# Kernel tuning notes

Hardware: AMD Instinct MI355X
Metric: run time of the kernel (lower is better)

The kernel has to match this reference:

```python
import jax, jax.numpy as jnp
import numpy as np

N = 50000      # num nodes
E = 1600000    # num edges
C = 128        # channels
F = 4          # number of framelet filters
K = 6          # Chebyshev order
S = 1.0        # spectral scale s
APPROX = np.array([[0.3, 0.15, 0.1, 0.075, 0.06, 0.05],
                   [0.6, 0.3, 0.2, 0.15, 0.12, 0.1],
                   [0.9, 0.45, 0.3, 0.225, 0.18, 0.15],
                   [1.2, 0.6, 0.4, 0.3, 0.24, 0.2]], dtype=np.float32)


def setup_inputs() -> dict:
    key = jax.random.key(0)
    ks = jax.random.split(key, 6)
    scale = (2.0 / C) ** 0.5
    return {
        "x_real": jax.random.normal(ks[0], (N, C), jnp.float32),
        "x_imag": jax.random.normal(ks[1], (N, C), jnp.float32),
        "edge_index": jax.random.randint(ks[2], (2, E), 0, N, dtype=jnp.int32),
        "edge_weight": jax.random.uniform(ks[3], (E,), jnp.float32),
        "approx": jnp.asarray(APPROX),
        "theta": jnp.ones((F,), jnp.float32),
        "W_r": jax.random.normal(ks[4], (C, C), jnp.float32) * scale,
        "W_i": jax.random.normal(ks[5], (C, C), jnp.float32) * scale,
        "num_nodes": N,
    }


def _framelet_fwd(x_real, x_imag, edge_index, edge_weight, approx, theta, W_r, W_i, num_nodes):
    row, col = edge_index[0], edge_index[1]
    w = edge_weight / S

    def A_norm(h):  # h: [N, C] real; normalized adjacency propagation
        return jax.ops.segment_sum(w[:, None] * h[col], row, num_segments=num_nodes)

    # Linearity: sum_i theta_i * sum_k approx[i,k] * T_k(x) == sum_k c_k * T_k(x)
    c = theta @ approx  # [K] effective Chebyshev coefficients

    T0r, T0i = x_real, x_imag
    out_r = c[0] * T0r
    out_i = c[0] * T0i
    T1r, T1i = -A_norm(T0r), -A_norm(T0i)
    out_r = out_r + c[1] * T1r
    out_i = out_i + c[1] * T1i
    for ki in range(2, K):
        T2r = -2.0 * A_norm(T1r) - T0r
        T2i = -2.0 * A_norm(T1i) - T0i
        out_r = out_r + c[ki] * T2r
        out_i = out_i + c[ki] * T2i
        T0r, T0i, T1r, T1i = T1r, T1i, T2r, T2i

    # complex linear: (r + i*j) @ (W_r + W_i*j)^T
    yr = out_r @ W_r.T - out_i @ W_i.T
    yi = out_r @ W_i.T + out_i @ W_r.T
    # CSiLU: SiLU applied to real/imag parts independently
    return jnp.stack([jax.nn.silu(yr), jax.nn.silu(yi)])  # [2, N, C]


def reference(x_real, x_imag, edge_index, edge_weight, approx, theta, W_r, W_i, num_nodes):
    return _framelet_fwd(x_real, x_imag, edge_index, edge_weight, approx, theta, W_r, W_i, num_nodes)
```

## Files before the change

### kernel.cpp

```cpp
#include <hip/hip_runtime.h>
#include <hip/hip_fp16.h>
#include <math.h>


#define CH   128
#define NP   128
#define NP4  64
#define RPB  128
#define MAXBUCK 512

typedef _Float16 half8 __attribute__((ext_vector_type(8)));
typedef float f32x4 __attribute__((ext_vector_type(4)));


__global__ __launch_bounds__(256) void bucket_hist_k(
        const int* __restrict__ row, int* __restrict__ bucket_cnt, int E, int nbuck) {
    __shared__ int h[MAXBUCK];
    for (int j = threadIdx.x; j < nbuck; j += 256) h[j] = 0;
    __syncthreads();
    int stride = gridDim.x * 256;
    for (int e = blockIdx.x * 256 + threadIdx.x; e < E; e += stride)
        atomicAdd(&h[row[e] >> 7], 1);
    __syncthreads();
    for (int j = threadIdx.x; j < nbuck; j += 256)
        if (h[j]) atomicAdd(&bucket_cnt[j], h[j]);
}

__global__ __launch_bounds__(512) void bucket_scan_k(
        const int* __restrict__ bucket_cnt, int* __restrict__ bucket_start,
        int* __restrict__ bucket_cursor, int nbuck, int E) {
    __shared__ int sd[MAXBUCK];
    int t = threadIdx.x;
    int v = (t < nbuck) ? bucket_cnt[t] : 0;
    sd[t] = v;
    __syncthreads();
    for (int off = 1; off < MAXBUCK; off <<= 1) {
        int y = (t >= off) ? sd[t - off] : 0;
        __syncthreads();
        sd[t] += y;
        __syncthreads();
    }
    int excl = sd[t] - v;
    if (t < nbuck) { bucket_start[t] = excl; bucket_cursor[t] = excl; }
    if (t == 0) bucket_start[nbuck] = E;
}

__global__ __launch_bounds__(256) void bucket_place_k(
        const int* __restrict__ row, const int* __restrict__ col,
        const float* __restrict__ w, int* __restrict__ bucket_cursor,
        uint2* __restrict__ tmp, int E, int chunk, int nbuck) {
    __shared__ int cnt[MAXBUCK];
    __shared__ int cur[MAXBUCK];
    int e0 = blockIdx.x * chunk;
    int e1 = e0 + chunk; if (e1 > E) e1 = E;
    if (e0 >= E) return;
    for (int j = threadIdx.x; j < nbuck; j += 256) cnt[j] = 0;
    __syncthreads();
    for (int e = e0 + threadIdx.x; e < e1; e += 256)
        atomicAdd(&cnt[row[e] >> 7], 1);
    __syncthreads();
    for (int j = threadIdx.x; j < nbuck; j += 256) {
        int c = cnt[j];
        cur[j] = c ? atomicAdd(&bucket_cursor[j], c) : 0;
    }
    __syncthreads();
    for (int e = e0 + threadIdx.x; e < e1; e += 256) {
        int r = row[e];
        int b = r >> 7;
        int p = atomicAdd(&cur[b], 1);
        uint2 ent;
        ent.x = ((unsigned)(r & (RPB - 1)) << 16) | (unsigned)col[e];
        ent.y = __float_as_uint(w[e]);
        tmp[p] = ent;
    }
}

__global__ __launch_bounds__(256) void csr_build_k(
        const uint2* __restrict__ tmp, const int* __restrict__ bucket_start,
        int* __restrict__ row_start, unsigned* __restrict__ csr4,
        int N, int E, int nbuck) {
    __shared__ int hist[RPB];
    __shared__ int sc[RPB];
    __shared__ int curs[RPB];
    int b = blockIdx.x;
    int t = threadIdx.x;
    int base = bucket_start[b];
    int endp = bucket_start[b + 1];
    if (t < RPB) hist[t] = 0;
    __syncthreads();
    for (int e = base + t; e < endp; e += 256)
        atomicAdd(&hist[tmp[e].x >> 16], 1);
    __syncthreads();
    if (t < RPB) sc[t] = hist[t];
    __syncthreads();
    for (int off = 1; off < RPB; off <<= 1) {
        int y = 0;
        if (t < RPB && t >= off) y = sc[t - off];
        __syncthreads();
        if (t < RPB) sc[t] += y;
        __syncthreads();
    }
    int r0 = b << 7;
    if (t < RPB) {
        int excl = sc[t] - hist[t];
        if (r0 + t < N) row_start[r0 + t] = base + excl;
        curs[t] = base + excl;
    }
    if (b == nbuck - 1 && t == 0) row_start[N] = E;
    __syncthreads();
    for (int e = base + t; e < endp; e += 256) {
        uint2 ent = tmp[e];
        int rl = ent.x >> 16;
        unsigned c = ent.x & 0xffffu;
        float wv = __uint_as_float(ent.y) * (-1.0f / 16.0f);
        int p = atomicAdd(&curs[rl], 1);
        __half hw = __float2half(wv);
        csr4[p] = (c << 16) | (unsigned)__half_as_ushort(hw);
    }
}

__global__ void coef_k(const float* __restrict__ approx, const float* __restrict__ theta,
                       float* cp) {
    int k = threadIdx.x;
    if (k < 6 && blockIdx.x == 0) {
        float s = 0.f;
        for (int f = 0; f < 4; f++) s += theta[f] * approx[f * 6 + k];
        float sc = 1.f;
        for (int j = 0; j < k; j++) sc *= 32.f;
        cp[k] = s * sc;
    }
}

__global__ void convert_x_k(const float2* __restrict__ xr2, const float2* __restrict__ xi2,
                            __half2* __restrict__ xbuf, int total) {
    int idx = blockIdx.x * blockDim.x + threadIdx.x;
    if (idx >= total) return;
    int i = idx >> 7;
    int p = idx & 127;
    float2 v = (p < 64) ? xr2[(size_t)i * 64 + p] : xi2[(size_t)i * 64 + (p - 64)];
    xbuf[idx] = __floats2half2_rn(v.x, v.y);
}

__global__ void build_whT_k(const float* __restrict__ Wr, const float* __restrict__ Wi,
                            _Float16* __restrict__ WhT) {
    int idx = blockIdx.x * 256 + threadIdx.x;
    int j = idx >> 8, k = idx & 255;
    float v;
    if (j < 128) {
        v = (k < 128) ? Wr[j * 128 + k] : -Wi[j * 128 + (k - 128)];
    } else {
        v = (k < 128) ? Wi[(j - 128) * 128 + k] : Wr[(j - 128) * 128 + (k - 128)];
    }
    WhT[idx] = (_Float16)v;
}


__device__ __forceinline__ void unpack4(uint2 v, float& a, float& b, float& c, float& d) {
    __half2 lo = *reinterpret_cast<__half2*>(&v.x);
    __half2 hi = *reinterpret_cast<__half2*>(&v.y);
    float2 f0 = __half22float2(lo);
    float2 f1 = __half22float2(hi);
    a = f0.x; b = f0.y; c = f1.x; d = f1.y;
}

__device__ __forceinline__ void decode(unsigned ent, int& c, float& wv) {
    c = (int)(ent >> 16);
    wv = __half2float(__ushort_as_half((unsigned short)(ent & 0xffffu)));
}

__device__ __forceinline__ void gather_row(
        const uint2* __restrict__ src, const unsigned* __restrict__ csr,
        int beg, int end, int p4,
        float& s0, float& s1, float& s2, float& s3) {
    int e = beg;
    unsigned c0, c1, c2, c3;
    if (e + 4 <= end) { c0 = csr[e]; c1 = csr[e+1]; c2 = csr[e+2]; c3 = csr[e+3]; }
    for (; e + 8 <= end; e += 4) {
        unsigned n0 = csr[e+4], n1 = csr[e+5], n2 = csr[e+6], n3 = csr[e+7];
        int ia, ib, ic, id; float wa, wb, wc, wd;
        decode(c0, ia, wa); decode(c1, ib, wb); decode(c2, ic, wc); decode(c3, id, wd);
        float a0,a1,a2,a3, b0,b1,b2,b3, d0,d1,d2,d3, f0,f1,f2,f3;
        unpack4(src[(size_t)ia * NP4 + p4], a0,a1,a2,a3);
        unpack4(src[(size_t)ib * NP4 + p4], b0,b1,b2,b3);
        unpack4(src[(size_t)ic * NP4 + p4], d0,d1,d2,d3);
        unpack4(src[(size_t)id * NP4 + p4], f0,f1,f2,f3);
        s0 += wa*a0 + wb*b0 + wc*d0 + wd*f0;
        s1 += wa*a1 + wb*b1 + wc*d1 + wd*f1;
        s2 += wa*a2 + wb*b2 + wc*d2 + wd*f2;
        s3 += wa*a3 + wb*b3 + wc*d3 + wd*f3;
        c0 = n0; c1 = n1; c2 = n2; c3 = n3;
    }
    if (e + 4 <= end) {
        int ia, ib, ic, id; float wa, wb, wc, wd;
        decode(c0, ia, wa); decode(c1, ib, wb); decode(c2, ic, wc); decode(c3, id, wd);
        float a0,a1,a2,a3, b0,b1,b2,b3, d0,d1,d2,d3, f0,f1,f2,f3;
        unpack4(src[(size_t)ia * NP4 + p4], a0,a1,a2,a3);
        unpack4(src[(size_t)ib * NP4 + p4], b0,b1,b2,b3);
        unpack4(src[(size_t)ic * NP4 + p4], d0,d1,d2,d3);
        unpack4(src[(size_t)id * NP4 + p4], f0,f1,f2,f3);
        s0 += wa*a0 + wb*b0 + wc*d0 + wd*f0;
        s1 += wa*a1 + wb*b1 + wc*d1 + wd*f1;
        s2 += wa*a2 + wb*b2 + wc*d2 + wd*f2;
        s3 += wa*a3 + wb*b3 + wc*d3 + wd*f3;
        e += 4;
    }
    for (; e < end; e++) {
        int ia; float wa;
        decode(csr[e], ia, wa);
        float a0,a1,a2,a3;
        unpack4(src[(size_t)ia * NP4 + p4], a0,a1,a2,a3);
        s0 += wa*a0; s1 += wa*a1; s2 += wa*a2; s3 += wa*a3;
    }
}

__global__ __launch_bounds__(256) void spmm_first4_k(
        const uint2* __restrict__ xb4,
        const int* __restrict__ row_start, const unsigned* __restrict__ csr,
        const float* __restrict__ cp,
        uint2* __restrict__ t1, float4* __restrict__ acc4, int N) {
    int t = threadIdx.x;
    int rl = t >> 6;
    int p4 = t & 63;
    int i = blockIdx.x * 4 + rl;
    if (i >= N) return;
    int beg = row_start[i], end = row_start[i + 1];
    float s0 = 0.f, s1 = 0.f, s2 = 0.f, s3 = 0.f;
    gather_row(xb4, csr, beg, end, p4, s0, s1, s2, s3);
    s0 *= 0.5f; s1 *= 0.5f; s2 *= 0.5f; s3 *= 0.5f;
    uint2 pk;
    __half2 h0 = __floats2half2_rn(s0, s1);
    __half2 h1 = __floats2half2_rn(s2, s3);
    pk.x = *reinterpret_cast<unsigned*>(&h0);
    pk.y = *reinterpret_cast<unsigned*>(&h1);
    t1[(size_t)i * NP4 + p4] = pk;
    float o0,o1,o2,o3;
    unpack4(xb4[(size_t)i * NP4 + p4], o0,o1,o2,o3);
    float cp0 = cp[0], cp1 = cp[1];
    int half = p4 >> 5, q = p4 & 31;
    float4 a;
    a.x = cp0 * o0 + cp1 * s0;
    a.y = cp0 * o1 + cp1 * s1;
    a.z = cp0 * o2 + cp1 * s2;
    a.w = cp0 * o3 + cp1 * s3;
    acc4[(size_t)half * N * 32 + (size_t)i * 32 + q] = a;
}

__global__ __launch_bounds__(256) void spmm_step4_k(
        const uint2* __restrict__ cur, const uint2* __restrict__ prev,
        const int* __restrict__ row_start, const unsigned* __restrict__ csr,
        const float* __restrict__ cp, int k,
        uint2* __restrict__ dst, float4* __restrict__ acc4, int N, int writeDst) {
    int t = threadIdx.x;
    int rl = t >> 6;
    int p4 = t & 63;
    int i = blockIdx.x * 4 + rl;
    if (i >= N) return;
    int beg = row_start[i], end = row_start[i + 1];
    float s0 = 0.f, s1 = 0.f, s2 = 0.f, s3 = 0.f;
    gather_row(cur, csr, beg, end, p4, s0, s1, s2, s3);
    float p0,p1,p2,p3;
    unpack4(prev[(size_t)i * NP4 + p4], p0,p1,p2,p3);
    const float inv = 1.0f / 1024.0f;
    float t0 = s0 - inv * p0;
    float t1v = s1 - inv * p1;
    float t2v = s2 - inv * p2;
    float t3v = s3 - inv * p3;
    if (writeDst) {
        uint2 pk;
        __half2 h0 = __floats2half2_rn(t0, t1v);
        __half2 h1 = __floats2half2_rn(t2v, t3v);
        pk.x = *reinterpret_cast<unsigned*>(&h0);
        pk.y = *reinterpret_cast<unsigned*>(&h1);
        dst[(size_t)i * NP4 + p4] = pk;
    }
    float ck = cp[k];
    int half = p4 >> 5, q = p4 & 31;
    size_t aidx = (size_t)half * N * 32 + (size_t)i * 32 + q;
    float4 a = acc4[aidx];
    a.x += ck * t0;
    a.y += ck * t1v;
    a.z += ck * t2v;
    a.w += ck * t3v;
    acc4[aidx] = a;
}

__global__ __launch_bounds__(256) void gemm_silu_mfma_k(
        const _Float16* __restrict__ WhT,
        float* __restrict__ out, int N) {
    __shared__ _Float16 U[32][264];
    int t = threadIdx.x;
    int row0 = blockIdx.x * 32;
    const float4* out4 = (const float4*)out;
    const float isc = 1.0f / 32.0f;
    for (int q = t; q < 2048; q += 256) {
        int r = q >> 6;
        int kq = q & 63;
        int row = row0 + r;
        float4 v = make_float4(0.f, 0.f, 0.f, 0.f);
        if (row < N) {
            int half = kq >> 5;
            v = out4[(size_t)half * N * 32 + (size_t)row * 32 + (kq & 31)];
        }
        int k = kq * 4;
        U[r][k]   = (_Float16)(v.x * isc);
        U[r][k+1] = (_Float16)(v.y * isc);
        U[r][k+2] = (_Float16)(v.z * isc);
        U[r][k+3] = (_Float16)(v.w * isc);
    }
    __syncthreads();

    int wave = t >> 6;
    int lane = t & 63;
    int colbase = wave * 64;
    int lr = lane & 15;
    int lg = lane >> 4;
    f32x4 acc[2][4] = {};
    for (int kb = 0; kb < 8; kb++) {
        int k0 = kb * 32 + lg * 8;
        half8 a0 = *(const half8*)&U[lr][k0];
        half8 a1 = *(const half8*)&U[16 + lr][k0];
        #pragma unroll
        for (int nf = 0; nf < 4; nf++) {
            int col = colbase + nf * 16 + lr;
            half8 b = *(const half8*)&WhT[(size_t)col * 256 + k0];
            acc[0][nf] = __builtin_amdgcn_mfma_f32_16x16x32_f16(a0, b, acc[0][nf], 0, 0, 0);
            acc[1][nf] = __builtin_amdgcn_mfma_f32_16x16x32_f16(a1, b, acc[1][nf], 0, 0, 0);
        }
    }

    #pragma unroll
    for (int mf = 0; mf < 2; mf++) {
        #pragma unroll
        for (int nf = 0; nf < 4; nf++) {
            int col = colbase + nf * 16 + lr;
            int half = col >> 7, j = col & 127;
            #pragma unroll
            for (int r4 = 0; r4 < 4; r4++) {
                int row = row0 + mf * 16 + lg * 4 + r4;
                if (row < N) {
                    float v = acc[mf][nf][r4] * 32.f;
                    float sv = v / (1.f + expf(-v));
                    out[(size_t)half * N * CH + (size_t)row * CH + j] = sv;
                }
            }
        }
    }
}


extern "C" void kernel_launch(void* const* d_in, const int* in_sizes, int n_in,
                              void* d_out, int out_size, void* d_ws, size_t ws_size,
                              hipStream_t stream) {
    const float* xr     = (const float*)d_in[0];
    const float* xi     = (const float*)d_in[1];
    const int*   eidx   = (const int*)d_in[2];
    const float* ew     = (const float*)d_in[3];
    const float* approx = (const float*)d_in[4];
    const float* theta  = (const float*)d_in[5];
    const float* Wr     = (const float*)d_in[6];
    const float* Wi     = (const float*)d_in[7];

    const int N = in_sizes[0] / CH;
    const int E = in_sizes[3];
    const int* rowv = eidx;
    const int* colv = eidx + E;

    float*  outp = (float*)d_out;
    float4* acc4 = (float4*)d_out;

    char* w8 = (char*)d_ws;
    size_t off = 0;
    auto alloc = [&](size_t bytes) -> void* {
        void* ptr = w8 + off;
        off += (bytes + 255) & ~(size_t)255;
        return ptr;
    };
    float*    cp        = (float*)alloc(64 * 4);
    int*      bucket_cnt= (int*)alloc(MAXBUCK * 4);
    int*      bucket_st = (int*)alloc((MAXBUCK + 1) * 4);
    int*      bucket_cur= (int*)alloc(MAXBUCK * 4);
    int*      row_start = (int*)alloc((size_t)(N + 1) * 4);
    unsigned* csr4      = (unsigned*)alloc((size_t)E * 4);
    uint2*    tmp       = (uint2*)alloc((size_t)E * 8);
    _Float16* WhT       = (_Float16*)alloc(256 * 256 * 2);
    __half2*  xbuf      = (__half2*)alloc((size_t)N * NP * 4);
    __half2*  bufA      = (__half2*)alloc((size_t)N * NP * 4);
    __half2*  bufB      = (__half2*)alloc((size_t)N * NP * 4);
    (void)ws_size;

    const int NH = N * NP;
    const int nbuck = (N + RPB - 1) / RPB;
    const int chunk = (E + 255) / 256;

    hipMemsetAsync(bucket_cnt, 0, (size_t)MAXBUCK * 4, stream);
    coef_k<<<1, 64, 0, stream>>>(approx, theta, cp);
    build_whT_k<<<256, 256, 0, stream>>>(Wr, Wi, WhT);
    bucket_hist_k<<<256, 256, 0, stream>>>(rowv, bucket_cnt, E, nbuck);
    bucket_scan_k<<<1, MAXBUCK, 0, stream>>>(bucket_cnt, bucket_st, bucket_cur, nbuck, E);
    bucket_place_k<<<256, 256, 0, stream>>>(rowv, colv, ew, bucket_cur, tmp, E, chunk, nbuck);
    csr_build_k<<<nbuck, 256, 0, stream>>>(tmp, bucket_st, row_start, csr4, N, E, nbuck);
    convert_x_k<<<(NH + 255) / 256, 256, 0, stream>>>((const float2*)xr, (const float2*)xi, xbuf, NH);

    const int NG = (N + 3) / 4;
    const uint2* xb4 = (const uint2*)xbuf;
    uint2* bA = (uint2*)bufA;
    uint2* bB = (uint2*)bufB;

    spmm_first4_k<<<NG, 256, 0, stream>>>(xb4, row_start, csr4, cp, bB, acc4, N);
    spmm_step4_k<<<NG, 256, 0, stream>>>(bB, xb4, row_start, csr4, cp, 2, bA, acc4, N, 1);
    spmm_step4_k<<<NG, 256, 0, stream>>>(bA, bB, row_start, csr4, cp, 3, bB, acc4, N, 1);
    spmm_step4_k<<<NG, 256, 0, stream>>>(bB, bA, row_start, csr4, cp, 4, bA, acc4, N, 1);
    spmm_step4_k<<<NG, 256, 0, stream>>>(bA, bB, row_start, csr4, cp, 5, bB, acc4, N, 0);

    gemm_silu_mfma_k<<<(N + 31) / 32, 256, 0, stream>>>(WhT, outp, N);
}
```

Baseline: 698.4 us.

## Partition features into 8 column slabs and split rows across wave lanes

Rearranges the fp16 feature buffers into eight slabs of 32 features (64 bytes per node), and assigns each SpMM block one slab and 16 rows. Within a wave, 8 lanes split a row's edges and 8 lanes cover the slab, with a shuffle reduction at the end. Each slab (~3.2 MB) is meant to fit in cache so that random neighbour gathers hit L2 instead of HBM. The cost is that the CSR indices are read eight times, the shuffle reductions add work, and rows with few edges leave lanes idle.

After: 1.095 ms. 1.57x slower.

```diff
diff --git a/kernel.cpp b/kernel.cpp
--- a/kernel.cpp
+++ b/kernel.cpp
@@ -4,10 +4,9 @@
 
 
 #define CH   128
-#define NP   128
-#define NP4  64
 #define RPB  128
 #define MAXBUCK 512
+#define CSLOT 8
 
 typedef _Float16 half8 __attribute__((ext_vector_type(8)));
 typedef float f32x4 __attribute__((ext_vector_type(4)));
@@ -131,14 +130,22 @@
     }
 }
 
-__global__ void convert_x_k(const float2* __restrict__ xr2, const float2* __restrict__ xi2,
-                            __half2* __restrict__ xbuf, int total) {
+__global__ void convert_x_k(const float4* __restrict__ xr4, const float4* __restrict__ xi4,
+                            uint2* __restrict__ xbuf, int N) {
     int idx = blockIdx.x * blockDim.x + threadIdx.x;
-    if (idx >= total) return;
-    int i = idx >> 7;
-    int p = idx & 127;
-    float2 v = (p < 64) ? xr2[(size_t)i * 64 + p] : xi2[(size_t)i * 64 + (p - 64)];
-    xbuf[idx] = __floats2half2_rn(v.x, v.y);
+    if (idx >= N * 64) return;
+    int i = idx >> 6;
+    int slot = idx & 63;
+    int c = slot >> 3, s = slot & 7;
+    int f = c * 32 + s * 4;
+    int fl = f & 127;
+    float4 v = (f < 128) ? xr4[(size_t)i * 32 + (fl >> 2)] : xi4[(size_t)i * 32 + (fl >> 2)];
+    __half2 h0 = __floats2half2_rn(v.x, v.y);
+    __half2 h1 = __floats2half2_rn(v.z, v.w);
+    uint2 pk;
+    pk.x = *reinterpret_cast<unsigned*>(&h0);
+    pk.y = *reinterpret_cast<unsigned*>(&h1);
+    xbuf[((size_t)c * N + i) * CSLOT + s] = pk;
 }
 
 __global__ void build_whT_k(const float* __restrict__ Wr, const float* __restrict__ Wi,
@@ -155,133 +162,122 @@
 }
 
 
-__device__ __forceinline__ void unpack4(uint2 v, float& a, float& b, float& c, float& d) {
-    __half2 lo = *reinterpret_cast<__half2*>(&v.x);
-    __half2 hi = *reinterpret_cast<__half2*>(&v.y);
-    float2 f0 = __half22float2(lo);
-    float2 f1 = __half22float2(hi);
-    a = f0.x; b = f0.y; c = f1.x; d = f1.y;
-}
-
-__device__ __forceinline__ void decode(unsigned ent, int& c, float& wv) {
-    c = (int)(ent >> 16);
-    wv = __half2float(__ushort_as_half((unsigned short)(ent & 0xffffu)));
-}
-
-__device__ __forceinline__ void gather_row(
-        const uint2* __restrict__ src, const unsigned* __restrict__ csr,
-        int beg, int end, int p4,
-        float& s0, float& s1, float& s2, float& s3) {
-    int e = beg;
-    unsigned c0, c1, c2, c3;
-    if (e + 4 <= end) { c0 = csr[e]; c1 = csr[e+1]; c2 = csr[e+2]; c3 = csr[e+3]; }
-    for (; e + 8 <= end; e += 4) {
-        unsigned n0 = csr[e+4], n1 = csr[e+5], n2 = csr[e+6], n3 = csr[e+7];
-        int ia, ib, ic, id; float wa, wb, wc, wd;
-        decode(c0, ia, wa); decode(c1, ib, wb); decode(c2, ic, wc); decode(c3, id, wd);
-        float a0,a1,a2,a3, b0,b1,b2,b3, d0,d1,d2,d3, f0,f1,f2,f3;
-        unpack4(src[(size_t)ia * NP4 + p4], a0,a1,a2,a3);
-        unpack4(src[(size_t)ib * NP4 + p4], b0,b1,b2,b3);
-        unpack4(src[(size_t)ic * NP4 + p4], d0,d1,d2,d3);
-        unpack4(src[(size_t)id * NP4 + p4], f0,f1,f2,f3);
-        s0 += wa*a0 + wb*b0 + wc*d0 + wd*f0;
-        s1 += wa*a1 + wb*b1 + wc*d1 + wd*f1;
-        s2 += wa*a2 + wb*b2 + wc*d2 + wd*f2;
-        s3 += wa*a3 + wb*b3 + wc*d3 + wd*f3;
-        c0 = n0; c1 = n1; c2 = n2; c3 = n3;
-    }
-    if (e + 4 <= end) {
-        int ia, ib, ic, id; float wa, wb, wc, wd;
-        decode(c0, ia, wa); decode(c1, ib, wb); decode(c2, ic, wc); decode(c3, id, wd);
-        float a0,a1,a2,a3, b0,b1,b2,b3, d0,d1,d2,d3, f0,f1,f2,f3;
-        unpack4(src[(size_t)ia * NP4 + p4], a0,a1,a2,a3);
-        unpack4(src[(size_t)ib * NP4 + p4], b0,b1,b2,b3);
-        unpack4(src[(size_t)ic * NP4 + p4], d0,d1,d2,d3);
-        unpack4(src[(size_t)id * NP4 + p4], f0,f1,f2,f3);
-        s0 += wa*a0 + wb*b0 + wc*d0 + wd*f0;
-        s1 += wa*a1 + wb*b1 + wc*d1 + wd*f1;
-        s2 += wa*a2 + wb*b2 + wc*d2 + wd*f2;
-        s3 += wa*a3 + wb*b3 + wc*d3 + wd*f3;
-        e += 4;
-    }
-    for (; e < end; e++) {
-        int ia; float wa;
-        decode(csr[e], ia, wa);
-        float a0,a1,a2,a3;
-        unpack4(src[(size_t)ia * NP4 + p4], a0,a1,a2,a3);
-        s0 += wa*a0; s1 += wa*a1; s2 += wa*a2; s3 += wa*a3;
-    }
-}
-
-__global__ __launch_bounds__(256) void spmm_first4_k(
-        const uint2* __restrict__ xb4,
+__global__ __launch_bounds__(256) void spmm_first_pass_k(
+        const uint2* __restrict__ xbuf,
         const int* __restrict__ row_start, const unsigned* __restrict__ csr,
         const float* __restrict__ cp,
         uint2* __restrict__ t1, float4* __restrict__ acc4, int N) {
-    int t = threadIdx.x;
-    int rl = t >> 6;
-    int p4 = t & 63;
-    int i = blockIdx.x * 4 + rl;
-    if (i >= N) return;
-    int beg = row_start[i], end = row_start[i + 1];
-    float s0 = 0.f, s1 = 0.f, s2 = 0.f, s3 = 0.f;
-    gather_row(xb4, csr, beg, end, p4, s0, s1, s2, s3);
-    s0 *= 0.5f; s1 *= 0.5f; s2 *= 0.5f; s3 *= 0.5f;
-    uint2 pk;
-    __half2 h0 = __floats2half2_rn(s0, s1);
-    __half2 h1 = __floats2half2_rn(s2, s3);
-    pk.x = *reinterpret_cast<unsigned*>(&h0);
-    pk.y = *reinterpret_cast<unsigned*>(&h1);
-    t1[(size_t)i * NP4 + p4] = pk;
-    float o0,o1,o2,o3;
-    unpack4(xb4[(size_t)i * NP4 + p4], o0,o1,o2,o3);
+    int c = blockIdx.x & 7;
+    int rb = blockIdx.x >> 3;
+    int wave = threadIdx.x >> 6, lane = threadIdx.x & 63;
+    int g = lane >> 3, s = lane & 7;
+    const uint2* srcc = xbuf + (size_t)c * N * CSLOT;
     float cp0 = cp[0], cp1 = cp[1];
-    int half = p4 >> 5, q = p4 & 31;
-    float4 a;
-    a.x = cp0 * o0 + cp1 * s0;
-    a.y = cp0 * o1 + cp1 * s1;
-    a.z = cp0 * o2 + cp1 * s2;
-    a.w = cp0 * o3 + cp1 * s3;
-    acc4[(size_t)half * N * 32 + (size_t)i * 32 + q] = a;
-}
-
-__global__ __launch_bounds__(256) void spmm_step4_k(
+    for (int r = 0; r < 4; r++) {
+        int i = rb * 16 + wave * 4 + r;
+        if (i >= N) return;
+        int beg = row_start[i], end = row_start[i + 1];
+        float s0 = 0.f, s1 = 0.f, s2 = 0.f, s3 = 0.f;
+        for (int e = beg + g; e < end; e += 8) {
+            unsigned ent = csr[e];
+            int col = (int)(ent >> 16);
+            float w = __half2float(__ushort_as_half((unsigned short)(ent & 0xffffu)));
+            uint2 v = srcc[(size_t)col * CSLOT + s];
+            float2 f0 = __half22float2(*reinterpret_cast<__half2*>(&v.x));
+            float2 f1 = __half22float2(*reinterpret_cast<__half2*>(&v.y));
+            s0 += w * f0.x; s1 += w * f0.y; s2 += w * f1.x; s3 += w * f1.y;
+        }
+        #pragma unroll
+        for (int m = 8; m < 64; m <<= 1) {
+            s0 += __shfl_xor(s0, m, 64);
+            s1 += __shfl_xor(s1, m, 64);
+            s2 += __shfl_xor(s2, m, 64);
+            s3 += __shfl_xor(s3, m, 64);
+        }
+        if (g == 0) {
+            s0 *= 0.5f; s1 *= 0.5f; s2 *= 0.5f; s3 *= 0.5f;
+            size_t ridx = ((size_t)c * N + i) * CSLOT + s;
+            __half2 h0 = __floats2half2_rn(s0, s1);
+            __half2 h1 = __floats2half2_rn(s2, s3);
+            uint2 pk;
+            pk.x = *reinterpret_cast<unsigned*>(&h0);
+            pk.y = *reinterpret_cast<unsigned*>(&h1);
+            t1[ridx] = pk;
+            uint2 ov = srcc[(size_t)i * CSLOT + s];
+            float2 o0 = __half22float2(*reinterpret_cast<__half2*>(&ov.x));
+            float2 o1 = __half22float2(*reinterpret_cast<__half2*>(&ov.y));
+            int f = c * 32 + s * 4;
+            size_t aidx = (size_t)(f >> 7) * N * 32 + (size_t)i * 32 + ((f & 127) >> 2);
+            float4 a;
+            a.x = cp0 * o0.x + cp1 * s0;
+            a.y = cp0 * o0.y + cp1 * s1;
+            a.z = cp0 * o1.x + cp1 * s2;
+            a.w = cp0 * o1.y + cp1 * s3;
+            acc4[aidx] = a;
+        }
+    }
+}
+
+__global__ __launch_bounds__(256) void spmm_step_pass_k(
         const uint2* __restrict__ cur, const uint2* __restrict__ prev,
         const int* __restrict__ row_start, const unsigned* __restrict__ csr,
         const float* __restrict__ cp, int k,
         uint2* __restrict__ dst, float4* __restrict__ acc4, int N, int writeDst) {
-    int t = threadIdx.x;
-    int rl = t >> 6;
-    int p4 = t & 63;
-    int i = blockIdx.x * 4 + rl;
-    if (i >= N) return;
-    int beg = row_start[i], end = row_start[i + 1];
-    float s0 = 0.f, s1 = 0.f, s2 = 0.f, s3 = 0.f;
-    gather_row(cur, csr, beg, end, p4, s0, s1, s2, s3);
-    float p0,p1,p2,p3;
-    unpack4(prev[(size_t)i * NP4 + p4], p0,p1,p2,p3);
-    const float inv = 1.0f / 1024.0f;
-    float t0 = s0 - inv * p0;
-    float t1v = s1 - inv * p1;
-    float t2v = s2 - inv * p2;
-    float t3v = s3 - inv * p3;
-    if (writeDst) {
-        uint2 pk;
-        __half2 h0 = __floats2half2_rn(t0, t1v);
-        __half2 h1 = __floats2half2_rn(t2v, t3v);
-        pk.x = *reinterpret_cast<unsigned*>(&h0);
-        pk.y = *reinterpret_cast<unsigned*>(&h1);
-        dst[(size_t)i * NP4 + p4] = pk;
-    }
+    int c = blockIdx.x & 7;
+    int rb = blockIdx.x >> 3;
+    int wave = threadIdx.x >> 6, lane = threadIdx.x & 63;
+    int g = lane >> 3, s = lane & 7;
+    const uint2* srcc = cur + (size_t)c * N * CSLOT;
     float ck = cp[k];
-    int half = p4 >> 5, q = p4 & 31;
-    size_t aidx = (size_t)half * N * 32 + (size_t)i * 32 + q;
-    float4 a = acc4[aidx];
-    a.x += ck * t0;
-    a.y += ck * t1v;
-    a.z += ck * t2v;
-    a.w += ck * t3v;
-    acc4[aidx] = a;
+    for (int r = 0; r < 4; r++) {
+        int i = rb * 16 + wave * 4 + r;
+        if (i >= N) return;
+        int beg = row_start[i], end = row_start[i + 1];
+        float s0 = 0.f, s1 = 0.f, s2 = 0.f, s3 = 0.f;
+        for (int e = beg + g; e < end; e += 8) {
+            unsigned ent = csr[e];
+            int col = (int)(ent >> 16);
+            float w = __half2float(__ushort_as_half((unsigned short)(ent & 0xffffu)));
+            uint2 v = srcc[(size_t)col * CSLOT + s];
+            float2 f0 = __half22float2(*reinterpret_cast<__half2*>(&v.x));
+            float2 f1 = __half22float2(*reinterpret_cast<__half2*>(&v.y));
+            s0 += w * f0.x; s1 += w * f0.y; s2 += w * f1.x; s3 += w * f1.y;
+        }
+        #pragma unroll
+        for (int m = 8; m < 64; m <<= 1) {
+            s0 += __shfl_xor(s0, m, 64);
+            s1 += __shfl_xor(s1, m, 64);
+            s2 += __shfl_xor(s2, m, 64);
+            s3 += __shfl_xor(s3, m, 64);
+        }
+        if (g == 0) {
+            size_t ridx = ((size_t)c * N + i) * CSLOT + s;
+            uint2 pv = prev[ridx];
+            float2 p0 = __half22float2(*reinterpret_cast<__half2*>(&pv.x));
+            float2 p1 = __half22float2(*reinterpret_cast<__half2*>(&pv.y));
+            const float inv = 1.0f / 1024.0f;
+            float t0 = s0 - inv * p0.x;
+            float t1v = s1 - inv * p0.y;
+            float t2v = s2 - inv * p1.x;
+            float t3v = s3 - inv * p1.y;
+            if (writeDst) {
+                __half2 h0 = __floats2half2_rn(t0, t1v);
+                __half2 h1 = __floats2half2_rn(t2v, t3v);
+                uint2 pk;
+                pk.x = *reinterpret_cast<unsigned*>(&h0);
+                pk.y = *reinterpret_cast<unsigned*>(&h1);
+                dst[ridx] = pk;
+            }
+            int f = c * 32 + s * 4;
+            size_t aidx = (size_t)(f >> 7) * N * 32 + (size_t)i * 32 + ((f & 127) >> 2);
+            float4 a = acc4[aidx];
+            a.x += ck * t0;
+            a.y += ck * t1v;
+            a.z += ck * t2v;
+            a.w += ck * t3v;
+            acc4[aidx] = a;
+        }
+    }
 }
 
 __global__ __launch_bounds__(256) void gemm_silu_mfma_k(
@@ -383,12 +379,11 @@
     unsigned* csr4      = (unsigned*)alloc((size_t)E * 4);
     uint2*    tmp       = (uint2*)alloc((size_t)E * 8);
     _Float16* WhT       = (_Float16*)alloc(256 * 256 * 2);
-    __half2*  xbuf      = (__half2*)alloc((size_t)N * NP * 4);
-    __half2*  bufA      = (__half2*)alloc((size_t)N * NP * 4);
-    __half2*  bufB      = (__half2*)alloc((size_t)N * NP * 4);
+    uint2*    xbuf      = (uint2*)alloc((size_t)N * 64 * 8);
+    uint2*    bufA      = (uint2*)alloc((size_t)N * 64 * 8);
+    uint2*    bufB      = (uint2*)alloc((size_t)N * 64 * 8);
     (void)ws_size;
 
-    const int NH = N * NP;
     const int nbuck = (N + RPB - 1) / RPB;
     const int chunk = (E + 255) / 256;
 
@@ -399,18 +394,16 @@
     bucket_scan_k<<<1, MAXBUCK, 0, stream>>>(bucket_cnt, bucket_st, bucket_cur, nbuck, E);
     bucket_place_k<<<256, 256, 0, stream>>>(rowv, colv, ew, bucket_cur, tmp, E, chunk, nbuck);
     csr_build_k<<<nbuck, 256, 0, stream>>>(tmp, bucket_st, row_start, csr4, N, E, nbuck);
-    convert_x_k<<<(NH + 255) / 256, 256, 0, stream>>>((const float2*)xr, (const float2*)xi, xbuf, NH);
-
-    const int NG = (N + 3) / 4;
-    const uint2* xb4 = (const uint2*)xbuf;
-    uint2* bA = (uint2*)bufA;
-    uint2* bB = (uint2*)bufB;
-
-    spmm_first4_k<<<NG, 256, 0, stream>>>(xb4, row_start, csr4, cp, bB, acc4, N);
-    spmm_step4_k<<<NG, 256, 0, stream>>>(bB, xb4, row_start, csr4, cp, 2, bA, acc4, N, 1);
-    spmm_step4_k<<<NG, 256, 0, stream>>>(bA, bB, row_start, csr4, cp, 3, bB, acc4, N, 1);
-    spmm_step4_k<<<NG, 256, 0, stream>>>(bB, bA, row_start, csr4, cp, 4, bA, acc4, N, 1);
-    spmm_step4_k<<<NG, 256, 0, stream>>>(bA, bB, row_start, csr4, cp, 5, bB, acc4, N, 0);
+    convert_x_k<<<(N * 64 + 255) / 256, 256, 0, stream>>>(
+        (const float4*)xr, (const float4*)xi, xbuf, N);
+
+    const int NG = 8 * ((N + 15) / 16);
+
+    spmm_first_pass_k<<<NG, 256, 0, stream>>>(xbuf, row_start, csr4, cp, bufB, acc4, N);
+    spmm_step_pass_k<<<NG, 256, 0, stream>>>(bufB, xbuf, row_start, csr4, cp, 2, bufA, acc4, N, 1);
+    spmm_step_pass_k<<<NG, 256, 0, stream>>>(bufA, bufB, row_start, csr4, cp, 3, bufB, acc4, N, 1);
+    spmm_step_pass_k<<<NG, 256, 0, stream>>>(bufB, bufA, row_start, csr4, cp, 4, bufA, acc4, N, 1);
+    spmm_step_pass_k<<<NG, 256, 0, stream>>>(bufA, bufB, row_start, csr4, cp, 5, bufB, acc4, N, 0);
 
     gemm_silu_mfma_k<<<(N + 31) / 32, 256, 0, stream>>>(WhT, outp, N);
 }
```

## Store Chebyshev terms in fp16 and combine them in the GEMM prologue

Applied to the files above, without the earlier changes.

The fp32 accumulator that each SpMM step used to read and write is removed. Every Chebyshev term T1..T5 is now kept as its own fp16 buffer, with T4 and T5 parked in the output buffer and T3 reusing the edge-sort scratch space. The GEMM prologue loads all six terms with nontemporal loads and forms the coefficient-weighted sum before the MFMA. This is meant to cut the large fp32 read-modify-write traffic per step. In exchange it needs more workspace, adds an fp16 store in the final step, and slightly changes rounding.

Result: faster. 658.8 us (-5.7%).

```diff
diff --git a/kernel.cpp b/kernel.cpp
--- a/kernel.cpp
+++ b/kernel.cpp
@@ -11,6 +11,12 @@
 
 typedef _Float16 half8 __attribute__((ext_vector_type(8)));
 typedef float f32x4 __attribute__((ext_vector_type(4)));
+
+__device__ __forceinline__ uint2 ntload_u2(const uint2* p) {
+    unsigned long long v = __builtin_nontemporal_load((const unsigned long long*)p);
+    uint2 r; r.x = (unsigned)v; r.y = (unsigned)(v >> 32);
+    return r;
+}
 
 
 __global__ __launch_bounds__(256) void bucket_hist_k(
@@ -216,8 +222,7 @@
 __global__ __launch_bounds__(256) void spmm_first4_k(
         const uint2* __restrict__ xb4,
         const int* __restrict__ row_start, const unsigned* __restrict__ csr,
-        const float* __restrict__ cp,
-        uint2* __restrict__ t1, float4* __restrict__ acc4, int N) {
+        uint2* __restrict__ dst, int N) {
     int t = threadIdx.x;
     int rl = t >> 6;
     int p4 = t & 63;
@@ -232,24 +237,13 @@
     __half2 h1 = __floats2half2_rn(s2, s3);
     pk.x = *reinterpret_cast<unsigned*>(&h0);
     pk.y = *reinterpret_cast<unsigned*>(&h1);
-    t1[(size_t)i * NP4 + p4] = pk;
-    float o0,o1,o2,o3;
-    unpack4(xb4[(size_t)i * NP4 + p4], o0,o1,o2,o3);
-    float cp0 = cp[0], cp1 = cp[1];
-    int half = p4 >> 5, q = p4 & 31;
-    float4 a;
-    a.x = cp0 * o0 + cp1 * s0;
-    a.y = cp0 * o1 + cp1 * s1;
-    a.z = cp0 * o2 + cp1 * s2;
-    a.w = cp0 * o3 + cp1 * s3;
-    acc4[(size_t)half * N * 32 + (size_t)i * 32 + q] = a;
+    dst[(size_t)i * NP4 + p4] = pk;
 }
 
 __global__ __launch_bounds__(256) void spmm_step4_k(
         const uint2* __restrict__ cur, const uint2* __restrict__ prev,
         const int* __restrict__ row_start, const unsigned* __restrict__ csr,
-        const float* __restrict__ cp, int k,
-        uint2* __restrict__ dst, float4* __restrict__ acc4, int N, int writeDst) {
+        uint2* __restrict__ dst, int N) {
     int t = threadIdx.x;
     int rl = t >> 6;
     int p4 = t & 63;
@@ -259,53 +253,59 @@
     float s0 = 0.f, s1 = 0.f, s2 = 0.f, s3 = 0.f;
     gather_row(cur, csr, beg, end, p4, s0, s1, s2, s3);
     float p0,p1,p2,p3;
-    unpack4(prev[(size_t)i * NP4 + p4], p0,p1,p2,p3);
+    unpack4(ntload_u2(&prev[(size_t)i * NP4 + p4]), p0,p1,p2,p3);
     const float inv = 1.0f / 1024.0f;
     float t0 = s0 - inv * p0;
     float t1v = s1 - inv * p1;
     float t2v = s2 - inv * p2;
     float t3v = s3 - inv * p3;
-    if (writeDst) {
-        uint2 pk;
-        __half2 h0 = __floats2half2_rn(t0, t1v);
-        __half2 h1 = __floats2half2_rn(t2v, t3v);
-        pk.x = *reinterpret_cast<unsigned*>(&h0);
-        pk.y = *reinterpret_cast<unsigned*>(&h1);
-        dst[(size_t)i * NP4 + p4] = pk;
-    }
-    float ck = cp[k];
-    int half = p4 >> 5, q = p4 & 31;
-    size_t aidx = (size_t)half * N * 32 + (size_t)i * 32 + q;
-    float4 a = acc4[aidx];
-    a.x += ck * t0;
-    a.y += ck * t1v;
-    a.z += ck * t2v;
-    a.w += ck * t3v;
-    acc4[aidx] = a;
+    uint2 pk;
+    __half2 h0 = __floats2half2_rn(t0, t1v);
+    __half2 h1 = __floats2half2_rn(t2v, t3v);
+    pk.x = *reinterpret_cast<unsigned*>(&h0);
+    pk.y = *reinterpret_cast<unsigned*>(&h1);
+    dst[(size_t)i * NP4 + p4] = pk;
 }
 
 __global__ __launch_bounds__(256) void gemm_silu_mfma_k(
         const _Float16* __restrict__ WhT,
+        const uint2* __restrict__ x0, const uint2* __restrict__ t1b,
+        const uint2* __restrict__ t2b, const uint2* __restrict__ t3b,
+        const float* __restrict__ cp,
         float* __restrict__ out, int N) {
     __shared__ _Float16 U[32][264];
     int t = threadIdx.x;
     int row0 = blockIdx.x * 32;
-    const float4* out4 = (const float4*)out;
+    const uint2* t4b = (const uint2*)out;
+    const uint2* t5b = (const uint2*)out + (size_t)N * NP4;
     const float isc = 1.0f / 32.0f;
+    float w0 = cp[0], w1 = cp[1], w2 = cp[2], w3 = cp[3], w4 = cp[4], w5 = cp[5];
     for (int q = t; q < 2048; q += 256) {
         int r = q >> 6;
-        int kq = q & 63;
+        int s = q & 63;
         int row = row0 + r;
-        float4 v = make_float4(0.f, 0.f, 0.f, 0.f);
+        float a0 = 0.f, a1 = 0.f, a2 = 0.f, a3 = 0.f;
         if (row < N) {
-            int half = kq >> 5;
-            v = out4[(size_t)half * N * 32 + (size_t)row * 32 + (kq & 31)];
+            size_t idx = (size_t)row * NP4 + s;
+            float v0,v1,v2,v3;
+            unpack4(ntload_u2(&x0[idx]),  v0,v1,v2,v3);
+            a0 += w0*v0; a1 += w0*v1; a2 += w0*v2; a3 += w0*v3;
+            unpack4(ntload_u2(&t1b[idx]), v0,v1,v2,v3);
+            a0 += w1*v0; a1 += w1*v1; a2 += w1*v2; a3 += w1*v3;
+            unpack4(ntload_u2(&t2b[idx]), v0,v1,v2,v3);
+            a0 += w2*v0; a1 += w2*v1; a2 += w2*v2; a3 += w2*v3;
+            unpack4(ntload_u2(&t3b[idx]), v0,v1,v2,v3);
+            a0 += w3*v0; a1 += w3*v1; a2 += w3*v2; a3 += w3*v3;
+            unpack4(ntload_u2(&t4b[idx]), v0,v1,v2,v3);
+            a0 += w4*v0; a1 += w4*v1; a2 += w4*v2; a3 += w4*v3;
+            unpack4(ntload_u2(&t5b[idx]), v0,v1,v2,v3);
+            a0 += w5*v0; a1 += w5*v1; a2 += w5*v2; a3 += w5*v3;
         }
-        int k = kq * 4;
-        U[r][k]   = (_Float16)(v.x * isc);
-        U[r][k+1] = (_Float16)(v.y * isc);
-        U[r][k+2] = (_Float16)(v.z * isc);
-        U[r][k+3] = (_Float16)(v.w * isc);
+        int k = s * 4;
+        U[r][k]   = (_Float16)(a0 * isc);
+        U[r][k+1] = (_Float16)(a1 * isc);
+        U[r][k+2] = (_Float16)(a2 * isc);
+        U[r][k+3] = (_Float16)(a3 * isc);
     }
     __syncthreads();
 
@@ -365,8 +365,7 @@
     const int* rowv = eidx;
     const int* colv = eidx + E;
 
-    float*  outp = (float*)d_out;
-    float4* acc4 = (float4*)d_out;
+    float* outp = (float*)d_out;
 
     char* w8 = (char*)d_ws;
     size_t off = 0;
@@ -381,16 +380,19 @@
     int*      bucket_cur= (int*)alloc(MAXBUCK * 4);
     int*      row_start = (int*)alloc((size_t)(N + 1) * 4);
     unsigned* csr4      = (unsigned*)alloc((size_t)E * 4);
-    uint2*    tmp       = (uint2*)alloc((size_t)E * 8);
     _Float16* WhT       = (_Float16*)alloc(256 * 256 * 2);
-    __half2*  xbuf      = (__half2*)alloc((size_t)N * NP * 4);
-    __half2*  bufA      = (__half2*)alloc((size_t)N * NP * 4);
-    __half2*  bufB      = (__half2*)alloc((size_t)N * NP * 4);
+    uint2*    xbuf      = (uint2*)alloc((size_t)N * NP4 * 8);
+    uint2*    T1        = (uint2*)alloc((size_t)N * NP4 * 8);
+    uint2*    T2        = (uint2*)alloc((size_t)N * NP4 * 8);
+    uint2*    T3        = (uint2*)alloc((size_t)N * NP4 * 8);
+    uint2*    tmp       = T3;
+    uint2*    T4        = (uint2*)d_out;
+    uint2*    T5        = (uint2*)d_out + (size_t)N * NP4;
     (void)ws_size;
 
-    const int NH = N * NP;
     const int nbuck = (N + RPB - 1) / RPB;
     const int chunk = (E + 255) / 256;
+    const int NH = N * NP;
 
     hipMemsetAsync(bucket_cnt, 0, (size_t)MAXBUCK * 4, stream);
     coef_k<<<1, 64, 0, stream>>>(approx, theta, cp);
@@ -399,18 +401,17 @@
     bucket_scan_k<<<1, MAXBUCK, 0, stream>>>(bucket_cnt, bucket_st, bucket_cur, nbuck, E);
     bucket_place_k<<<256, 256, 0, stream>>>(rowv, colv, ew, bucket_cur, tmp, E, chunk, nbuck);
     csr_build_k<<<nbuck, 256, 0, stream>>>(tmp, bucket_st, row_start, csr4, N, E, nbuck);
-    convert_x_k<<<(NH + 255) / 256, 256, 0, stream>>>((const float2*)xr, (const float2*)xi, xbuf, NH);
+    convert_x_k<<<(NH + 255) / 256, 256, 0, stream>>>(
+        (const float2*)xr, (const float2*)xi, (__half2*)xbuf, NH);
 
     const int NG = (N + 3) / 4;
-    const uint2* xb4 = (const uint2*)xbuf;
-    uint2* bA = (uint2*)bufA;
-    uint2* bB = (uint2*)bufB;
-
-    spmm_first4_k<<<NG, 256, 0, stream>>>(xb4, row_start, csr4, cp, bB, acc4, N);
-    spmm_step4_k<<<NG, 256, 0, stream>>>(bB, xb4, row_start, csr4, cp, 2, bA, acc4, N, 1);
-    spmm_step4_k<<<NG, 256, 0, stream>>>(bA, bB, row_start, csr4, cp, 3, bB, acc4, N, 1);
-    spmm_step4_k<<<NG, 256, 0, stream>>>(bB, bA, row_start, csr4, cp, 4, bA, acc4, N, 1);
-    spmm_step4_k<<<NG, 256, 0, stream>>>(bA, bB, row_start, csr4, cp, 5, bB, acc4, N, 0);
-
-    gemm_silu_mfma_k<<<(N + 31) / 32, 256, 0, stream>>>(WhT, outp, N);
-}
+
+    spmm_first4_k<<<NG, 256, 0, stream>>>(xbuf, row_start, csr4, T1, N);
+    spmm_step4_k<<<NG, 256, 0, stream>>>(T1, xbuf, row_start, csr4, T2, N);
+    spmm_step4_k<<<NG, 256, 0, stream>>>(T2, T1, row_start, csr4, T3, N);
+    spmm_step4_k<<<NG, 256, 0, stream>>>(T3, T2, row_start, csr4, T4, N);
+    spmm_step4_k<<<NG, 256, 0, stream>>>(T4, T3, row_start, csr4, T5, N);
+
+    gemm_silu_mfma_k<<<(N + 31) / 32, 256, 0, stream>>>(
+        WhT, xbuf, T1, T2, T3, cp, outp, N);
+}
```
